# Kernel tuning notes

Hardware: AMD Instinct MI355X
Metric: run time of the kernel (lower is better)

Reference implementation:

```python
import jax, jax.numpy as jnp
import numpy as np

N_SRC = 100000
N_DST = 100000
D = 128
K = 10
E_SAMP = 1000000


def setup_inputs() -> dict:
    key = jax.random.key(0)
    k1, k2, k3, k4, k5, k6, k7 = jax.random.split(key, 7)
    h_src = jax.random.normal(k1, (N_SRC, D), dtype=jnp.float32)
    weight = jax.random.normal(k2, (D, D), dtype=jnp.float32) * (1.0 / np.sqrt(D))
    bias = jax.random.normal(k3, (D,), dtype=jnp.float32) * 0.01
    sampled_src = jax.random.randint(k4, (E_SAMP,), 0, N_SRC, dtype=jnp.int64)
    sampled_dst = jnp.sort(jax.random.randint(k5, (E_SAMP,), 0, N_DST, dtype=jnp.int64))
    out_deg = jax.random.randint(k6, (N_SRC,), 0, 64, dtype=jnp.int32)
    in_deg = jax.random.randint(k7, (N_DST,), 0, 64, dtype=jnp.int32)
    return {
        "h_src": h_src,
        "weight": weight,
        "bias": bias,
        "sampled_src": sampled_src,
        "sampled_dst": sampled_dst,
        "out_deg": out_deg,
        "in_deg": in_deg,
    }


def reference(h_src, weight, bias, sampled_src, sampled_dst, out_deg, in_deg):
    # pre-aggregation normalization: out_degree^-0.5 (clamped to >=1)
    norm_src = jnp.clip(out_deg.astype(h_src.dtype), 1.0, None) ** -0.5  # [N_SRC]
    feat_src = h_src * norm_src[:, None]                                  # [N_SRC, D]
    # fused gather + (pre-sampled) neighbor sum: copy_src -> segment_sum
    msg = feat_src[sampled_src]                                           # [E_SAMP, D]
    agg = jax.ops.segment_sum(msg, sampled_dst, num_segments=N_DST,
                              indices_are_sorted=True)                    # [N_DST, D]
    rst = agg @ weight                                                    # [N_DST, D]
    # post normalization: clamp(in_degree, 1, k)^-0.5
    norm_dst = jnp.clip(in_deg.astype(rst.dtype), 1.0, float(K)) ** -0.5  # [N_DST]
    rst = rst * norm_dst[:, None] + bias
    return rst
```

## Files before the change

### kernel.cpp

```cpp
#include <hip/hip_runtime.h>
#include <hip/hip_bf16.h>
#include <cstdint>

#define NDIM 128
#define KCLAMP 10.0f

using bf16x8 = __attribute__((ext_vector_type(8))) short;
using f32x4  = __attribute__((ext_vector_type(4))) float;
using f32x2  = __attribute__((ext_vector_type(2))) float;

__device__ __forceinline__ uint16_t f2bf(float f) {
    uint32_t u = __float_as_uint(f);
    uint32_t r = (u + 0x7fffu + ((u >> 16) & 1u)) >> 16;
    return (uint16_t)r;
}
__device__ __forceinline__ float bf_lo(uint32_t v) { return __uint_as_float(v << 16); }
__device__ __forceinline__ float bf_hi(uint32_t v) { return __uint_as_float(v & 0xffff0000u); }

__global__ void k_feat(const float* __restrict__ h, const int* __restrict__ odeg,
                       uint16_t* __restrict__ feat, int nsrc) {
    int idx = blockIdx.x * blockDim.x + threadIdx.x;
    int total = nsrc * (NDIM / 4);
    if (idx >= total) return;
    int row = idx >> 5;
    float dg = (float)odeg[row];
    float nrm = rsqrtf(fmaxf(dg, 1.0f));
    float4 v = ((const float4*)h)[idx];
    ushort4 o;
    o.x = f2bf(v.x * nrm);
    o.y = f2bf(v.y * nrm);
    o.z = f2bf(v.z * nrm);
    o.w = f2bf(v.w * nrm);
    ((ushort4*)feat)[idx] = o;
}

__global__ void k_rowptr(const int* __restrict__ sdst, int E,
                         int* __restrict__ row_start, int ndst) {
    int d = blockIdx.x * blockDim.x + threadIdx.x;
    if (d > ndst) return;
    int lo = 0, hi = E;
    while (lo < hi) {
        int mid = (lo + hi) >> 1;
        if (sdst[mid] < d) lo = mid + 1; else hi = mid;
    }
    row_start[d] = lo;
}

__global__ void k_agg_bf(const uint16_t* __restrict__ feat,
                         const int* __restrict__ ssrc, const int* __restrict__ row_start,
                         uint16_t* __restrict__ agg, int ndst) {
    constexpr int U = 8;
    int gtid = blockIdx.x * blockDim.x + threadIdx.x;
    int wave = gtid >> 6;
    int lane = threadIdx.x & 63;
    int sub  = lane >> 4;
    int li   = lane & 15;
    int nwaves = (gridDim.x * blockDim.x) >> 6;

    for (int d0 = wave * 4; d0 < ndst; d0 += nwaves * 4) {
        int d = d0 + sub;
        int valid = (d < ndst);
        int s = 0, e = 0;
        if (valid) { s = row_start[d]; e = row_start[d + 1]; }
        int elast = (e > s) ? (e - 1) : 0;

        f32x2 acc[4];
#pragma unroll
        for (int k = 0; k < 4; ++k) acc[k] = (f32x2){0.f, 0.f};

        int idxv[U];
#pragma unroll
        for (int u = 0; u < U; ++u) idxv[u] = ssrc[min(s + u, elast)];

        int pos = s;
        while (__any(pos < e)) {
            uint4 v[U];
#pragma unroll
            for (int u = 0; u < U; ++u)
                v[u] = *(const uint4*)(feat + (size_t)idxv[u] * NDIM + li * 8);

            int npos = pos + U;
#pragma unroll
            for (int u = 0; u < U; ++u) idxv[u] = ssrc[min(npos + u, elast)];

#pragma unroll
            for (int u = 0; u < U; ++u) {
                if (pos + u < e) {
                    f32x2 t0 = {bf_lo(v[u].x), bf_hi(v[u].x)};
                    f32x2 t1 = {bf_lo(v[u].y), bf_hi(v[u].y)};
                    f32x2 t2 = {bf_lo(v[u].z), bf_hi(v[u].z)};
                    f32x2 t3 = {bf_lo(v[u].w), bf_hi(v[u].w)};
                    acc[0] += t0; acc[1] += t1; acc[2] += t2; acc[3] += t3;
                }
            }
            pos = npos;
        }

        if (valid) {
            uint4 o;
            o.x = (uint32_t)f2bf(acc[0][0]) | ((uint32_t)f2bf(acc[0][1]) << 16);
            o.y = (uint32_t)f2bf(acc[1][0]) | ((uint32_t)f2bf(acc[1][1]) << 16);
            o.z = (uint32_t)f2bf(acc[2][0]) | ((uint32_t)f2bf(acc[2][1]) << 16);
            o.w = (uint32_t)f2bf(acc[3][0]) | ((uint32_t)f2bf(acc[3][1]) << 16);
            *(uint4*)(agg + (size_t)d * NDIM + li * 8) = o;
        }
    }
}

__global__ void k_agg_f32(const uint16_t* __restrict__ feat,
                          const float* __restrict__ h, const int* __restrict__ odeg,
                          const int* __restrict__ ssrc, const int* __restrict__ row_start,
                          float* __restrict__ agg, int ndst, int use_feat) {
    int gtid = blockIdx.x * blockDim.x + threadIdx.x;
    int wave = gtid >> 6;
    int lane = threadIdx.x & 63;
    int nwaves = (gridDim.x * blockDim.x) >> 6;
    for (int d = wave; d < ndst; d += nwaves) {
        int s = row_start[d], e = row_start[d + 1];
        float a0 = 0.f, a1 = 0.f;
        if (use_feat) {
            for (int i = s; i < e; i++) {
                uint32_t v0 = *(const uint32_t*)(feat + (size_t)ssrc[i] * NDIM + lane * 2);
                a0 += bf_lo(v0);
                a1 += bf_hi(v0);
            }
        } else {
            for (int i = s; i < e; i++) {
                int s0 = ssrc[i];
                float nrm = rsqrtf(fmaxf((float)odeg[s0], 1.0f));
                float2 v = ((const float2*)h)[(size_t)s0 * (NDIM / 2) + lane];
                a0 += v.x * nrm;
                a1 += v.y * nrm;
            }
        }
        float2 o; o.x = a0; o.y = a1;
        ((float2*)agg)[(size_t)d * (NDIM / 2) + lane] = o;
    }
}

__global__ void k_wfrag(const float* __restrict__ W, uint16_t* __restrict__ wfrag) {
    int t = blockIdx.x * blockDim.x + threadIdx.x;
    if (t >= NDIM * NDIM) return;
    int i    = t & 7;
    int lane = (t >> 3) & 63;
    int s    = (t >> 9) & 3;
    int n    = t >> 11;
    int k    = s * 32 + 8 * (lane >> 4) + i;
    int col  = n * 16 + (lane & 15);
    wfrag[t] = f2bf(W[k * NDIM + col]);
}

__global__ __launch_bounds__(256) void k_gemm_mfma(const uint16_t* __restrict__ A,
                                                   const uint16_t* __restrict__ wfrag,
                                                   const float* __restrict__ bias,
                                                   const int* __restrict__ ideg,
                                                   float* __restrict__ out, int M) {
    __shared__ uint16_t Ws[NDIM * NDIM];
    int tx = threadIdx.x;
    for (int i = tx; i < NDIM * NDIM / 8; i += 256)
        ((int4*)Ws)[i] = ((const int4*)wfrag)[i];
    __syncthreads();

    int wave = tx >> 6, lane = tx & 63;
    int r0 = blockIdx.x * 64 + wave * 16;
    int arow = r0 + (lane & 15);
    if (arow >= M) arow = M - 1;
    const bf16x8* Arow = (const bf16x8*)(A + (size_t)arow * NDIM);
    int g = lane >> 4;

    f32x4 acc[8];
#pragma unroll
    for (int n = 0; n < 8; ++n) acc[n] = (f32x4){0.f, 0.f, 0.f, 0.f};

#pragma unroll
    for (int s = 0; s < 4; ++s) {
        bf16x8 af = Arow[s * 4 + g];
#pragma unroll
        for (int n = 0; n < 8; ++n) {
            bf16x8 bfr = *(const bf16x8*)(Ws + (((n * 4 + s) * 64 + lane) << 3));
            acc[n] = __builtin_amdgcn_mfma_f32_16x16x32_bf16(af, bfr, acc[n], 0, 0, 0);
        }
    }

    int col = lane & 15;
    float nrm[4];
    int rowbase = r0 + g * 4;
#pragma unroll
    for (int r = 0; r < 4; ++r) {
        int row = rowbase + r;
        nrm[r] = (row < M) ? rsqrtf(fminf(fmaxf((float)ideg[row], 1.0f), KCLAMP)) : 0.f;
    }
#pragma unroll
    for (int n = 0; n < 8; ++n) {
        float b = bias[n * 16 + col];
#pragma unroll
        for (int r = 0; r < 4; ++r) {
            int row = rowbase + r;
            if (row < M)
                out[(size_t)row * NDIM + n * 16 + col] = acc[n][r] * nrm[r] + b;
        }
    }
}

__global__ __launch_bounds__(256) void k_gemm_f32(float* __restrict__ io,
                                                  const float* __restrict__ W,
                                                  const float* __restrict__ bias,
                                                  const int* __restrict__ ideg, int M) {
    __shared__ float Wsf[NDIM][NDIM];
    int tx = threadIdx.x;
    {
        const float4* Wv = (const float4*)W;
        float4* Wsv = (float4*)&Wsf[0][0];
        for (int i = tx; i < NDIM * NDIM / 4; i += 256) Wsv[i] = Wv[i];
    }
    __syncthreads();
    int cg = tx & 31, rg = tx >> 5;
    int r0 = blockIdx.x * 64 + rg * 8, c0 = cg * 4;
    float acc[8][4];
#pragma unroll
    for (int r = 0; r < 8; ++r)
#pragma unroll
        for (int c = 0; c < 4; ++c) acc[r][c] = 0.f;
    for (int k4 = 0; k4 < NDIM / 4; ++k4) {
        float4 wk0 = *(const float4*)&Wsf[4 * k4 + 0][c0];
        float4 wk1 = *(const float4*)&Wsf[4 * k4 + 1][c0];
        float4 wk2 = *(const float4*)&Wsf[4 * k4 + 2][c0];
        float4 wk3 = *(const float4*)&Wsf[4 * k4 + 3][c0];
#pragma unroll
        for (int r = 0; r < 8; ++r) {
            int row = r0 + r;
            if (row < M) {
                float4 a = ((const float4*)io)[(size_t)row * (NDIM / 4) + k4];
                acc[r][0] += a.x * wk0.x + a.y * wk1.x + a.z * wk2.x + a.w * wk3.x;
                acc[r][1] += a.x * wk0.y + a.y * wk1.y + a.z * wk2.y + a.w * wk3.y;
                acc[r][2] += a.x * wk0.z + a.y * wk1.z + a.z * wk2.z + a.w * wk3.z;
                acc[r][3] += a.x * wk0.w + a.y * wk1.w + a.z * wk2.w + a.w * wk3.w;
            }
        }
    }
    __syncthreads();
    float4 b = *(const float4*)&bias[c0];
#pragma unroll
    for (int r = 0; r < 8; ++r) {
        int row = r0 + r;
        if (row < M) {
            float nrm = rsqrtf(fminf(fmaxf((float)ideg[row], 1.0f), KCLAMP));
            float4 o;
            o.x = acc[r][0] * nrm + b.x;
            o.y = acc[r][1] * nrm + b.y;
            o.z = acc[r][2] * nrm + b.z;
            o.w = acc[r][3] * nrm + b.w;
            ((float4*)io)[(size_t)row * (NDIM / 4) + cg] = o;
        }
    }
}

extern "C" void kernel_launch(void* const* d_in, const int* in_sizes, int n_in,
                              void* d_out, int out_size, void* d_ws, size_t ws_size,
                              hipStream_t stream) {
    const float* h_src  = (const float*)d_in[0];
    const float* weight = (const float*)d_in[1];
    const float* bias   = (const float*)d_in[2];
    const int*   ssrc   = (const int*)d_in[3];
    const int*   sdst   = (const int*)d_in[4];
    const int*   odeg   = (const int*)d_in[5];
    const int*   ideg   = (const int*)d_in[6];
    float* out = (float*)d_out;

    int E    = in_sizes[3];
    int nsrc = in_sizes[0] / NDIM;
    int ndst = out_size / NDIM;

    size_t featB = (size_t)nsrc * NDIM * 2;
    size_t aggB  = (size_t)ndst * NDIM * 2;

    int*      row_start = (int*)d_ws;
    uint16_t* wfrag = (uint16_t*)((char*)d_ws + ((size_t)1 << 20));
    size_t feat_off = (size_t)2 << 20;
    uint16_t* feat  = (uint16_t*)((char*)d_ws + feat_off);
    size_t agg_off  = feat_off + ((featB + 255) & ~(size_t)255);
    uint16_t* aggbf = (uint16_t*)((char*)d_ws + agg_off);
    size_t need_full = agg_off + aggB;
    size_t need_feat = feat_off + featB;

    k_rowptr<<<(ndst + 1 + 255) / 256, 256, 0, stream>>>(sdst, E, row_start, ndst);

    if (ws_size >= need_full) {
        k_wfrag<<<(NDIM * NDIM + 255) / 256, 256, 0, stream>>>(weight, wfrag);
        int total = nsrc * (NDIM / 4);
        k_feat<<<(total + 255) / 256, 256, 0, stream>>>(h_src, odeg, feat, nsrc);
        k_agg_bf<<<2048, 256, 0, stream>>>(feat, ssrc, row_start, aggbf, ndst);
        k_gemm_mfma<<<(ndst + 63) / 64, 256, 0, stream>>>(aggbf, wfrag,
                                                          bias, ideg, out, ndst);
    } else {
        int use_feat = (ws_size >= need_feat) ? 1 : 0;
        if (use_feat) {
            int total = nsrc * (NDIM / 4);
            k_feat<<<(total + 255) / 256, 256, 0, stream>>>(h_src, odeg, feat, nsrc);
        }
        k_agg_f32<<<2048, 256, 0, stream>>>(feat, h_src, odeg, ssrc, row_start, out, ndst, use_feat);
        k_gemm_f32<<<(ndst + 63) / 64, 256, 0, stream>>>(out, weight, bias, ideg, ndst);
    }
}
```

Baseline: 86.54 us.

## Fuse aggregation with MFMA GEMM and merge prep kernels into one launch

Merges the feature-normalization, row-pointer binary search and weight-fragment kernels into a single block-partitioned prep launch. Fuses the bf16 neighbor aggregation into the MFMA GEMM: each 512-thread block aggregates 128 destination rows into a swizzled LDS tile, then multiplies it by the LDS-resident weights. This removes the bf16 agg round-trip through global memory and two launches. In exchange it uses 64KB of LDS per block and a fixed-size grid without grid-stride, which lowers occupancy and latency hiding for the gather.

Measured after the change: 83.42 us. 1.04x faster.

```diff
diff --git a/kernel.cpp b/kernel.cpp
--- a/kernel.cpp
+++ b/kernel.cpp
@@ -4,6 +4,7 @@
 
 #define NDIM 128
 #define KCLAMP 10.0f
+#define BLK_D 128
 
 using bf16x8 = __attribute__((ext_vector_type(8))) short;
 using f32x4  = __attribute__((ext_vector_type(4))) float;
@@ -17,48 +18,73 @@
 __device__ __forceinline__ float bf_lo(uint32_t v) { return __uint_as_float(v << 16); }
 __device__ __forceinline__ float bf_hi(uint32_t v) { return __uint_as_float(v & 0xffff0000u); }
 
-__global__ void k_feat(const float* __restrict__ h, const int* __restrict__ odeg,
-                       uint16_t* __restrict__ feat, int nsrc) {
-    int idx = blockIdx.x * blockDim.x + threadIdx.x;
-    int total = nsrc * (NDIM / 4);
-    if (idx >= total) return;
-    int row = idx >> 5;
-    float dg = (float)odeg[row];
-    float nrm = rsqrtf(fmaxf(dg, 1.0f));
-    float4 v = ((const float4*)h)[idx];
-    ushort4 o;
-    o.x = f2bf(v.x * nrm);
-    o.y = f2bf(v.y * nrm);
-    o.z = f2bf(v.z * nrm);
-    o.w = f2bf(v.w * nrm);
-    ((ushort4*)feat)[idx] = o;
-}
-
-__global__ void k_rowptr(const int* __restrict__ sdst, int E,
-                         int* __restrict__ row_start, int ndst) {
-    int d = blockIdx.x * blockDim.x + threadIdx.x;
-    if (d > ndst) return;
-    int lo = 0, hi = E;
-    while (lo < hi) {
-        int mid = (lo + hi) >> 1;
-        if (sdst[mid] < d) lo = mid + 1; else hi = mid;
-    }
-    row_start[d] = lo;
-}
-
-__global__ void k_agg_bf(const uint16_t* __restrict__ feat,
-                         const int* __restrict__ ssrc, const int* __restrict__ row_start,
-                         uint16_t* __restrict__ agg, int ndst) {
+__global__ void k_prep(const float* __restrict__ h, const int* __restrict__ odeg,
+                       uint16_t* __restrict__ feat, int nsrc,
+                       const int* __restrict__ sdst, int E,
+                       int* __restrict__ row_start, int ndst,
+                       const float* __restrict__ W, uint16_t* __restrict__ wfrag,
+                       int featBlocks, int rpBlocks) {
+    int b = blockIdx.x;
+    int tid = threadIdx.x;
+    if (b < featBlocks) {
+        int idx = b * 256 + tid;
+        int total = nsrc * (NDIM / 4);
+        if (idx >= total) return;
+        int row = idx >> 5;
+        float nrm = rsqrtf(fmaxf((float)odeg[row], 1.0f));
+        float4 v = ((const float4*)h)[idx];
+        ushort4 o;
+        o.x = f2bf(v.x * nrm);
+        o.y = f2bf(v.y * nrm);
+        o.z = f2bf(v.z * nrm);
+        o.w = f2bf(v.w * nrm);
+        ((ushort4*)feat)[idx] = o;
+    } else if (b < featBlocks + rpBlocks) {
+        int d = (b - featBlocks) * 256 + tid;
+        if (d > ndst) return;
+        int lo = 0, hi = E;
+        while (lo < hi) {
+            int mid = (lo + hi) >> 1;
+            if (sdst[mid] < d) lo = mid + 1; else hi = mid;
+        }
+        row_start[d] = lo;
+    } else {
+        int t = (b - featBlocks - rpBlocks) * 256 + tid;
+        if (t >= NDIM * NDIM) return;
+        int i    = t & 7;
+        int lane = (t >> 3) & 63;
+        int s    = (t >> 9) & 3;
+        int n    = t >> 11;
+        int k    = s * 32 + 8 * (lane >> 4) + i;
+        int col  = n * 16 + (lane & 15);
+        wfrag[t] = f2bf(W[k * NDIM + col]);
+    }
+}
+
+__global__ __launch_bounds__(512) void k_fused(const uint16_t* __restrict__ feat,
+                                               const int* __restrict__ ssrc,
+                                               const int* __restrict__ row_start,
+                                               const uint16_t* __restrict__ wfrag,
+                                               const float* __restrict__ bias,
+                                               const int* __restrict__ ideg,
+                                               float* __restrict__ out, int ndst) {
     constexpr int U = 8;
-    int gtid = blockIdx.x * blockDim.x + threadIdx.x;
-    int wave = gtid >> 6;
-    int lane = threadIdx.x & 63;
+    __shared__ uint16_t Ws[NDIM * NDIM];
+    __shared__ uint16_t Asm[BLK_D * NDIM];
+
+    int tx = threadIdx.x;
+    for (int i = tx; i < NDIM * NDIM / 8; i += 512)
+        ((int4*)Ws)[i] = ((const int4*)wfrag)[i];
+
+    int wave = tx >> 6, lane = tx & 63;
     int sub  = lane >> 4;
     int li   = lane & 15;
-    int nwaves = (gridDim.x * blockDim.x) >> 6;
-
-    for (int d0 = wave * 4; d0 < ndst; d0 += nwaves * 4) {
-        int d = d0 + sub;
+    int sid  = wave * 4 + sub;
+    int base = blockIdx.x * BLK_D;
+
+    for (int j = 0; j < 4; ++j) {
+        int r = sid * 4 + j;
+        int d = base + r;
         int valid = (d < ndst);
         int s = 0, e = 0;
         if (valid) { s = row_start[d]; e = row_start[d + 1]; }
@@ -96,15 +122,81 @@
             pos = npos;
         }
 
-        if (valid) {
-            uint4 o;
-            o.x = (uint32_t)f2bf(acc[0][0]) | ((uint32_t)f2bf(acc[0][1]) << 16);
-            o.y = (uint32_t)f2bf(acc[1][0]) | ((uint32_t)f2bf(acc[1][1]) << 16);
-            o.z = (uint32_t)f2bf(acc[2][0]) | ((uint32_t)f2bf(acc[2][1]) << 16);
-            o.w = (uint32_t)f2bf(acc[3][0]) | ((uint32_t)f2bf(acc[3][1]) << 16);
-            *(uint4*)(agg + (size_t)d * NDIM + li * 8) = o;
-        }
-    }
+        uint4 o;
+        o.x = (uint32_t)f2bf(acc[0][0]) | ((uint32_t)f2bf(acc[0][1]) << 16);
+        o.y = (uint32_t)f2bf(acc[1][0]) | ((uint32_t)f2bf(acc[1][1]) << 16);
+        o.z = (uint32_t)f2bf(acc[2][0]) | ((uint32_t)f2bf(acc[2][1]) << 16);
+        o.w = (uint32_t)f2bf(acc[3][0]) | ((uint32_t)f2bf(acc[3][1]) << 16);
+        int byte = (r * 256 + li * 16) ^ ((r & 7) << 4);
+        *(uint4*)((char*)Asm + byte) = o;
+    }
+
+    __syncthreads();
+
+    int g = lane >> 4;
+    int rloc = wave * 16 + (lane & 15);
+
+    f32x4 acc[8];
+#pragma unroll
+    for (int n = 0; n < 8; ++n) acc[n] = (f32x4){0.f, 0.f, 0.f, 0.f};
+
+#pragma unroll
+    for (int s = 0; s < 4; ++s) {
+        int abyte = (rloc * 256 + s * 64 + g * 16) ^ ((rloc & 7) << 4);
+        bf16x8 af = *(const bf16x8*)((const char*)Asm + abyte);
+#pragma unroll
+        for (int n = 0; n < 8; ++n) {
+            bf16x8 bfr = *(const bf16x8*)(Ws + (((n * 4 + s) * 64 + lane) << 3));
+            acc[n] = __builtin_amdgcn_mfma_f32_16x16x32_bf16(af, bfr, acc[n], 0, 0, 0);
+        }
+    }
+
+    int col = lane & 15;
+    int rowbase = base + wave * 16 + g * 4;
+    float nrm[4];
+#pragma unroll
+    for (int r = 0; r < 4; ++r) {
+        int row = rowbase + r;
+        nrm[r] = (row < ndst) ? rsqrtf(fminf(fmaxf((float)ideg[row], 1.0f), KCLAMP)) : 0.f;
+    }
+#pragma unroll
+    for (int n = 0; n < 8; ++n) {
+        float b = bias[n * 16 + col];
+#pragma unroll
+        for (int r = 0; r < 4; ++r) {
+            int row = rowbase + r;
+            if (row < ndst)
+                out[(size_t)row * NDIM + n * 16 + col] = acc[n][r] * nrm[r] + b;
+        }
+    }
+}
+
+__global__ void k_rowptr(const int* __restrict__ sdst, int E,
+                         int* __restrict__ row_start, int ndst) {
+    int d = blockIdx.x * blockDim.x + threadIdx.x;
+    if (d > ndst) return;
+    int lo = 0, hi = E;
+    while (lo < hi) {
+        int mid = (lo + hi) >> 1;
+        if (sdst[mid] < d) lo = mid + 1; else hi = mid;
+    }
+    row_start[d] = lo;
+}
+
+__global__ void k_feat(const float* __restrict__ h, const int* __restrict__ odeg,
+                       uint16_t* __restrict__ feat, int nsrc) {
+    int idx = blockIdx.x * blockDim.x + threadIdx.x;
+    int total = nsrc * (NDIM / 4);
+    if (idx >= total) return;
+    int row = idx >> 5;
+    float nrm = rsqrtf(fmaxf((float)odeg[row], 1.0f));
+    float4 v = ((const float4*)h)[idx];
+    ushort4 o;
+    o.x = f2bf(v.x * nrm);
+    o.y = f2bf(v.y * nrm);
+    o.z = f2bf(v.z * nrm);
+    o.w = f2bf(v.w * nrm);
+    ((ushort4*)feat)[idx] = o;
 }
 
 __global__ void k_agg_f32(const uint16_t* __restrict__ feat,
@@ -138,70 +230,6 @@
     }
 }
 
-__global__ void k_wfrag(const float* __restrict__ W, uint16_t* __restrict__ wfrag) {
-    int t = blockIdx.x * blockDim.x + threadIdx.x;
-    if (t >= NDIM * NDIM) return;
-    int i    = t & 7;
-    int lane = (t >> 3) & 63;
-    int s    = (t >> 9) & 3;
-    int n    = t >> 11;
-    int k    = s * 32 + 8 * (lane >> 4) + i;
-    int col  = n * 16 + (lane & 15);
-    wfrag[t] = f2bf(W[k * NDIM + col]);
-}
-
-__global__ __launch_bounds__(256) void k_gemm_mfma(const uint16_t* __restrict__ A,
-                                                   const uint16_t* __restrict__ wfrag,
-                                                   const float* __restrict__ bias,
-                                                   const int* __restrict__ ideg,
-                                                   float* __restrict__ out, int M) {
-    __shared__ uint16_t Ws[NDIM * NDIM];
-    int tx = threadIdx.x;
-    for (int i = tx; i < NDIM * NDIM / 8; i += 256)
-        ((int4*)Ws)[i] = ((const int4*)wfrag)[i];
-    __syncthreads();
-
-    int wave = tx >> 6, lane = tx & 63;
-    int r0 = blockIdx.x * 64 + wave * 16;
-    int arow = r0 + (lane & 15);
-    if (arow >= M) arow = M - 1;
-    const bf16x8* Arow = (const bf16x8*)(A + (size_t)arow * NDIM);
-    int g = lane >> 4;
-
-    f32x4 acc[8];
-#pragma unroll
-    for (int n = 0; n < 8; ++n) acc[n] = (f32x4){0.f, 0.f, 0.f, 0.f};
-
-#pragma unroll
-    for (int s = 0; s < 4; ++s) {
-        bf16x8 af = Arow[s * 4 + g];
-#pragma unroll
-        for (int n = 0; n < 8; ++n) {
-            bf16x8 bfr = *(const bf16x8*)(Ws + (((n * 4 + s) * 64 + lane) << 3));
-            acc[n] = __builtin_amdgcn_mfma_f32_16x16x32_bf16(af, bfr, acc[n], 0, 0, 0);
-        }
-    }
-
-    int col = lane & 15;
-    float nrm[4];
-    int rowbase = r0 + g * 4;
-#pragma unroll
-    for (int r = 0; r < 4; ++r) {
-        int row = rowbase + r;
-        nrm[r] = (row < M) ? rsqrtf(fminf(fmaxf((float)ideg[row], 1.0f), KCLAMP)) : 0.f;
-    }
-#pragma unroll
-    for (int n = 0; n < 8; ++n) {
-        float b = bias[n * 16 + col];
-#pragma unroll
-        for (int r = 0; r < 4; ++r) {
-            int row = rowbase + r;
-            if (row < M)
-                out[(size_t)row * NDIM + n * 16 + col] = acc[n][r] * nrm[r] + b;
-        }
-    }
-}
-
 __global__ __launch_bounds__(256) void k_gemm_f32(float* __restrict__ io,
                                                   const float* __restrict__ W,
                                                   const float* __restrict__ bias,
@@ -272,33 +300,25 @@
     int ndst = out_size / NDIM;
 
     size_t featB = (size_t)nsrc * NDIM * 2;
-    size_t aggB  = (size_t)ndst * NDIM * 2;
 
     int*      row_start = (int*)d_ws;
     uint16_t* wfrag = (uint16_t*)((char*)d_ws + ((size_t)1 << 20));
     size_t feat_off = (size_t)2 << 20;
     uint16_t* feat  = (uint16_t*)((char*)d_ws + feat_off);
-    size_t agg_off  = feat_off + ((featB + 255) & ~(size_t)255);
-    uint16_t* aggbf = (uint16_t*)((char*)d_ws + agg_off);
-    size_t need_full = agg_off + aggB;
-    size_t need_feat = feat_off + featB;
-
-    k_rowptr<<<(ndst + 1 + 255) / 256, 256, 0, stream>>>(sdst, E, row_start, ndst);
-
-    if (ws_size >= need_full) {
-        k_wfrag<<<(NDIM * NDIM + 255) / 256, 256, 0, stream>>>(weight, wfrag);
-        int total = nsrc * (NDIM / 4);
-        k_feat<<<(total + 255) / 256, 256, 0, stream>>>(h_src, odeg, feat, nsrc);
-        k_agg_bf<<<2048, 256, 0, stream>>>(feat, ssrc, row_start, aggbf, ndst);
-        k_gemm_mfma<<<(ndst + 63) / 64, 256, 0, stream>>>(aggbf, wfrag,
-                                                          bias, ideg, out, ndst);
+    size_t need = feat_off + featB;
+
+    if (ws_size >= need) {
+        int featBlocks = (nsrc * (NDIM / 4) + 255) / 256;
+        int rpBlocks   = (ndst + 1 + 255) / 256;
+        int wfBlocks   = (NDIM * NDIM + 255) / 256;
+        k_prep<<<featBlocks + rpBlocks + wfBlocks, 256, 0, stream>>>(
+            h_src, odeg, feat, nsrc, sdst, E, row_start, ndst,
+            weight, wfrag, featBlocks, rpBlocks);
+        k_fused<<<(ndst + BLK_D - 1) / BLK_D, 512, 0, stream>>>(
+            feat, ssrc, row_start, wfrag, bias, ideg, out, ndst);
     } else {
-        int use_feat = (ws_size >= need_feat) ? 1 : 0;
-        if (use_feat) {
-            int total = nsrc * (NDIM / 4);
-            k_feat<<<(total + 255) / 256, 256, 0, stream>>>(h_src, odeg, feat, nsrc);
-        }
-        k_agg_f32<<<2048, 256, 0, stream>>>(feat, h_src, odeg, ssrc, row_start, out, ndst, use_feat);
+        k_rowptr<<<(ndst + 1 + 255) / 256, 256, 0, stream>>>(sdst, E, row_start, ndst);
+        k_agg_f32<<<2048, 256, 0, stream>>>(feat, h_src, odeg, ssrc, row_start, out, ndst, 0);
         k_gemm_f32<<<(ndst + 63) / 64, 256, 0, stream>>>(out, weight, bias, ideg, ndst);
     }
 }
```

## Transform source features before gathering and fuse normalization, GEMM and rowptr into one launch

Applied to the files above, without the earlier changes.

Uses linearity to reorder the math: each source row is scaled and multiplied by W first, then the transformed bf16 rows are gathered and segment-summed. The epilogue (in-degree norm and bias) moves into the gather kernel, which writes fp32 output directly. The row-pointer binary search shares the launch with the GEMM blocks, cutting five launches to two and dropping the intermediate feat and agg buffers. In exchange it rounds the per-edge transformed rows to bf16 before summation, which changes where rounding error accumulates.

Result: slower. 91.65 us (+5.9%).

```diff
diff --git a/kernel.cpp b/kernel.cpp
--- a/kernel.cpp
+++ b/kernel.cpp
@@ -17,38 +17,98 @@
 __device__ __forceinline__ float bf_lo(uint32_t v) { return __uint_as_float(v << 16); }
 __device__ __forceinline__ float bf_hi(uint32_t v) { return __uint_as_float(v & 0xffff0000u); }
 
-__global__ void k_feat(const float* __restrict__ h, const int* __restrict__ odeg,
-                       uint16_t* __restrict__ feat, int nsrc) {
-    int idx = blockIdx.x * blockDim.x + threadIdx.x;
-    int total = nsrc * (NDIM / 4);
-    if (idx >= total) return;
-    int row = idx >> 5;
-    float dg = (float)odeg[row];
-    float nrm = rsqrtf(fmaxf(dg, 1.0f));
-    float4 v = ((const float4*)h)[idx];
-    ushort4 o;
-    o.x = f2bf(v.x * nrm);
-    o.y = f2bf(v.y * nrm);
-    o.z = f2bf(v.z * nrm);
-    o.w = f2bf(v.w * nrm);
-    ((ushort4*)feat)[idx] = o;
-}
-
-__global__ void k_rowptr(const int* __restrict__ sdst, int E,
-                         int* __restrict__ row_start, int ndst) {
-    int d = blockIdx.x * blockDim.x + threadIdx.x;
-    if (d > ndst) return;
-    int lo = 0, hi = E;
-    while (lo < hi) {
-        int mid = (lo + hi) >> 1;
-        if (sdst[mid] < d) lo = mid + 1; else hi = mid;
-    }
-    row_start[d] = lo;
-}
-
-__global__ void k_agg_bf(const uint16_t* __restrict__ feat,
-                         const int* __restrict__ ssrc, const int* __restrict__ row_start,
-                         uint16_t* __restrict__ agg, int ndst) {
+__global__ __launch_bounds__(256) void k1_trans_rowptr(
+        const float* __restrict__ h, const int* __restrict__ odeg,
+        const float* __restrict__ W, uint16_t* __restrict__ trans, int M,
+        const int* __restrict__ sdst, int E, int* __restrict__ row_start, int ndst,
+        int gemmBlocks) {
+    int b = blockIdx.x;
+    int tx = threadIdx.x;
+
+    if (b >= gemmBlocks) {
+        int d = (b - gemmBlocks) * 256 + tx;
+        if (d > ndst) return;
+        int lo = 0, hi = E;
+        while (lo < hi) {
+            int mid = (lo + hi) >> 1;
+            if (sdst[mid] < d) lo = mid + 1; else hi = mid;
+        }
+        row_start[d] = lo;
+        return;
+    }
+
+    __shared__ uint16_t Ws[NDIM * NDIM];
+    __shared__ uint16_t Asm[64 * NDIM];
+
+    int r0 = b * 64;
+
+    for (int i = tx; i < 64 * (NDIM / 4); i += 256) {
+        int row_loc = i >> 5;
+        int col4    = i & 31;
+        int row = r0 + row_loc;
+        float4 v = {0.f, 0.f, 0.f, 0.f};
+        float nrm = 0.f;
+        if (row < M) {
+            v = ((const float4*)h)[(size_t)row * (NDIM / 4) + col4];
+            nrm = rsqrtf(fmaxf((float)odeg[row], 1.0f));
+        }
+        ushort4 o;
+        o.x = f2bf(v.x * nrm);
+        o.y = f2bf(v.y * nrm);
+        o.z = f2bf(v.z * nrm);
+        o.w = f2bf(v.w * nrm);
+        int byte = (row_loc * 256 + col4 * 8) ^ ((row_loc & 7) << 4);
+        *(ushort4*)((char*)Asm + byte) = o;
+    }
+
+    for (int t = tx; t < NDIM * NDIM; t += 256) {
+        int i    = t & 7;
+        int ln   = (t >> 3) & 63;
+        int s    = (t >> 9) & 3;
+        int n    = t >> 11;
+        int k    = s * 32 + 8 * (ln >> 4) + i;
+        int col  = n * 16 + (ln & 15);
+        Ws[t] = f2bf(W[k * NDIM + col]);
+    }
+    __syncthreads();
+
+    int wave = tx >> 6, lane = tx & 63;
+    int g = lane >> 4;
+    int rloc = wave * 16 + (lane & 15);
+
+    f32x4 acc[8];
+#pragma unroll
+    for (int n = 0; n < 8; ++n) acc[n] = (f32x4){0.f, 0.f, 0.f, 0.f};
+
+#pragma unroll
+    for (int s = 0; s < 4; ++s) {
+        int abyte = (rloc * 256 + s * 64 + g * 16) ^ ((rloc & 7) << 4);
+        bf16x8 af = *(const bf16x8*)((const char*)Asm + abyte);
+#pragma unroll
+        for (int n = 0; n < 8; ++n) {
+            bf16x8 bfr = *(const bf16x8*)(Ws + (((n * 4 + s) * 64 + lane) << 3));
+            acc[n] = __builtin_amdgcn_mfma_f32_16x16x32_bf16(af, bfr, acc[n], 0, 0, 0);
+        }
+    }
+
+    int colL = lane & 15;
+    int rowbase = r0 + wave * 16 + g * 4;
+#pragma unroll
+    for (int n = 0; n < 8; ++n) {
+#pragma unroll
+        for (int r = 0; r < 4; ++r) {
+            int row = rowbase + r;
+            if (row < M)
+                trans[(size_t)row * NDIM + n * 16 + colL] = f2bf(acc[n][r]);
+        }
+    }
+}
+
+__global__ __launch_bounds__(256) void k2_gather(
+        const uint16_t* __restrict__ trans,
+        const int* __restrict__ ssrc, const int* __restrict__ row_start,
+        const float* __restrict__ bias, const int* __restrict__ ideg,
+        float* __restrict__ out, int ndst) {
     constexpr int U = 8;
     int gtid = blockIdx.x * blockDim.x + threadIdx.x;
     int wave = gtid >> 6;
@@ -57,6 +117,9 @@
     int li   = lane & 15;
     int nwaves = (gridDim.x * blockDim.x) >> 6;
 
+    float4 b0 = ((const float4*)bias)[li * 2];
+    float4 b1 = ((const float4*)bias)[li * 2 + 1];
+
     for (int d0 = wave * 4; d0 < ndst; d0 += nwaves * 4) {
         int d = d0 + sub;
         int valid = (d < ndst);
@@ -77,7 +140,7 @@
             uint4 v[U];
 #pragma unroll
             for (int u = 0; u < U; ++u)
-                v[u] = *(const uint4*)(feat + (size_t)idxv[u] * NDIM + li * 8);
+                v[u] = *(const uint4*)(trans + (size_t)idxv[u] * NDIM + li * 8);
 
             int npos = pos + U;
 #pragma unroll
@@ -97,20 +160,37 @@
         }
 
         if (valid) {
-            uint4 o;
-            o.x = (uint32_t)f2bf(acc[0][0]) | ((uint32_t)f2bf(acc[0][1]) << 16);
-            o.y = (uint32_t)f2bf(acc[1][0]) | ((uint32_t)f2bf(acc[1][1]) << 16);
-            o.z = (uint32_t)f2bf(acc[2][0]) | ((uint32_t)f2bf(acc[2][1]) << 16);
-            o.w = (uint32_t)f2bf(acc[3][0]) | ((uint32_t)f2bf(acc[3][1]) << 16);
-            *(uint4*)(agg + (size_t)d * NDIM + li * 8) = o;
-        }
-    }
-}
-
-__global__ void k_agg_f32(const uint16_t* __restrict__ feat,
-                          const float* __restrict__ h, const int* __restrict__ odeg,
+            float nrm = rsqrtf(fminf(fmaxf((float)ideg[d], 1.0f), KCLAMP));
+            float4 o0, o1;
+            o0.x = acc[0][0] * nrm + b0.x;
+            o0.y = acc[0][1] * nrm + b0.y;
+            o0.z = acc[1][0] * nrm + b0.z;
+            o0.w = acc[1][1] * nrm + b0.w;
+            o1.x = acc[2][0] * nrm + b1.x;
+            o1.y = acc[2][1] * nrm + b1.y;
+            o1.z = acc[3][0] * nrm + b1.z;
+            o1.w = acc[3][1] * nrm + b1.w;
+            ((float4*)out)[(size_t)d * (NDIM / 4) + li * 2]     = o0;
+            ((float4*)out)[(size_t)d * (NDIM / 4) + li * 2 + 1] = o1;
+        }
+    }
+}
+
+__global__ void k_rowptr(const int* __restrict__ sdst, int E,
+                         int* __restrict__ row_start, int ndst) {
+    int d = blockIdx.x * blockDim.x + threadIdx.x;
+    if (d > ndst) return;
+    int lo = 0, hi = E;
+    while (lo < hi) {
+        int mid = (lo + hi) >> 1;
+        if (sdst[mid] < d) lo = mid + 1; else hi = mid;
+    }
+    row_start[d] = lo;
+}
+
+__global__ void k_agg_f32(const float* __restrict__ h, const int* __restrict__ odeg,
                           const int* __restrict__ ssrc, const int* __restrict__ row_start,
-                          float* __restrict__ agg, int ndst, int use_feat) {
+                          float* __restrict__ agg, int ndst) {
     int gtid = blockIdx.x * blockDim.x + threadIdx.x;
     int wave = gtid >> 6;
     int lane = threadIdx.x & 63;
@@ -118,87 +198,15 @@
     for (int d = wave; d < ndst; d += nwaves) {
         int s = row_start[d], e = row_start[d + 1];
         float a0 = 0.f, a1 = 0.f;
-        if (use_feat) {
-            for (int i = s; i < e; i++) {
-                uint32_t v0 = *(const uint32_t*)(feat + (size_t)ssrc[i] * NDIM + lane * 2);
-                a0 += bf_lo(v0);
-                a1 += bf_hi(v0);
-            }
-        } else {
-            for (int i = s; i < e; i++) {
-                int s0 = ssrc[i];
-                float nrm = rsqrtf(fmaxf((float)odeg[s0], 1.0f));
-                float2 v = ((const float2*)h)[(size_t)s0 * (NDIM / 2) + lane];
-                a0 += v.x * nrm;
-                a1 += v.y * nrm;
-            }
+        for (int i = s; i < e; i++) {
+            int s0 = ssrc[i];
+            float nrm = rsqrtf(fmaxf((float)odeg[s0], 1.0f));
+            float2 v = ((const float2*)h)[(size_t)s0 * (NDIM / 2) + lane];
+            a0 += v.x * nrm;
+            a1 += v.y * nrm;
         }
         float2 o; o.x = a0; o.y = a1;
         ((float2*)agg)[(size_t)d * (NDIM / 2) + lane] = o;
-    }
-}
-
-__global__ void k_wfrag(const float* __restrict__ W, uint16_t* __restrict__ wfrag) {
-    int t = blockIdx.x * blockDim.x + threadIdx.x;
-    if (t >= NDIM * NDIM) return;
-    int i    = t & 7;
-    int lane = (t >> 3) & 63;
-    int s    = (t >> 9) & 3;
-    int n    = t >> 11;
-    int k    = s * 32 + 8 * (lane >> 4) + i;
-    int col  = n * 16 + (lane & 15);
-    wfrag[t] = f2bf(W[k * NDIM + col]);
-}
-
-__global__ __launch_bounds__(256) void k_gemm_mfma(const uint16_t* __restrict__ A,
-                                                   const uint16_t* __restrict__ wfrag,
-                                                   const float* __restrict__ bias,
-                                                   const int* __restrict__ ideg,
-                                                   float* __restrict__ out, int M) {
-    __shared__ uint16_t Ws[NDIM * NDIM];
-    int tx = threadIdx.x;
-    for (int i = tx; i < NDIM * NDIM / 8; i += 256)
-        ((int4*)Ws)[i] = ((const int4*)wfrag)[i];
-    __syncthreads();
-
-    int wave = tx >> 6, lane = tx & 63;
-    int r0 = blockIdx.x * 64 + wave * 16;
-    int arow = r0 + (lane & 15);
-    if (arow >= M) arow = M - 1;
-    const bf16x8* Arow = (const bf16x8*)(A + (size_t)arow * NDIM);
-    int g = lane >> 4;
-
-    f32x4 acc[8];
-#pragma unroll
-    for (int n = 0; n < 8; ++n) acc[n] = (f32x4){0.f, 0.f, 0.f, 0.f};
-
-#pragma unroll
-    for (int s = 0; s < 4; ++s) {
-        bf16x8 af = Arow[s * 4 + g];
-#pragma unroll
-        for (int n = 0; n < 8; ++n) {
-            bf16x8 bfr = *(const bf16x8*)(Ws + (((n * 4 + s) * 64 + lane) << 3));
-            acc[n] = __builtin_amdgcn_mfma_f32_16x16x32_bf16(af, bfr, acc[n], 0, 0, 0);
-        }
-    }
-
-    int col = lane & 15;
-    float nrm[4];
-    int rowbase = r0 + g * 4;
-#pragma unroll
-    for (int r = 0; r < 4; ++r) {
-        int row = rowbase + r;
-        nrm[r] = (row < M) ? rsqrtf(fminf(fmaxf((float)ideg[row], 1.0f), KCLAMP)) : 0.f;
-    }
-#pragma unroll
-    for (int n = 0; n < 8; ++n) {
-        float b = bias[n * 16 + col];
-#pragma unroll
-        for (int r = 0; r < 4; ++r) {
-            int row = rowbase + r;
-            if (row < M)
-                out[(size_t)row * NDIM + n * 16 + col] = acc[n][r] * nrm[r] + b;
-        }
     }
 }
 
@@ -271,34 +279,20 @@
     int nsrc = in_sizes[0] / NDIM;
     int ndst = out_size / NDIM;
 
-    size_t featB = (size_t)nsrc * NDIM * 2;
-    size_t aggB  = (size_t)ndst * NDIM * 2;
-
     int*      row_start = (int*)d_ws;
-    uint16_t* wfrag = (uint16_t*)((char*)d_ws + ((size_t)1 << 20));
-    size_t feat_off = (size_t)2 << 20;
-    uint16_t* feat  = (uint16_t*)((char*)d_ws + feat_off);
-    size_t agg_off  = feat_off + ((featB + 255) & ~(size_t)255);
-    uint16_t* aggbf = (uint16_t*)((char*)d_ws + agg_off);
-    size_t need_full = agg_off + aggB;
-    size_t need_feat = feat_off + featB;
-
-    k_rowptr<<<(ndst + 1 + 255) / 256, 256, 0, stream>>>(sdst, E, row_start, ndst);
-
-    if (ws_size >= need_full) {
-        k_wfrag<<<(NDIM * NDIM + 255) / 256, 256, 0, stream>>>(weight, wfrag);
-        int total = nsrc * (NDIM / 4);
-        k_feat<<<(total + 255) / 256, 256, 0, stream>>>(h_src, odeg, feat, nsrc);
-        k_agg_bf<<<2048, 256, 0, stream>>>(feat, ssrc, row_start, aggbf, ndst);
-        k_gemm_mfma<<<(ndst + 63) / 64, 256, 0, stream>>>(aggbf, wfrag,
-                                                          bias, ideg, out, ndst);
+    uint16_t* trans = (uint16_t*)((char*)d_ws + ((size_t)1 << 20));
+    size_t need = ((size_t)1 << 20) + (size_t)nsrc * NDIM * 2;
+
+    if (ws_size >= need) {
+        int gemmBlocks = (nsrc + 63) / 64;
+        int rpBlocks   = (ndst + 1 + 255) / 256;
+        k1_trans_rowptr<<<gemmBlocks + rpBlocks, 256, 0, stream>>>(
+            h_src, odeg, weight, trans, nsrc,
+            sdst, E, row_start, ndst, gemmBlocks);
+        k2_gather<<<2048, 256, 0, stream>>>(trans, ssrc, row_start, bias, ideg, out, ndst);
     } else {
-        int use_feat = (ws_size >= need_feat) ? 1 : 0;
-        if (use_feat) {
-            int total = nsrc * (NDIM / 4);
-            k_feat<<<(total + 255) / 256, 256, 0, stream>>>(h_src, odeg, feat, nsrc);
-        }
-        k_agg_f32<<<2048, 256, 0, stream>>>(feat, h_src, odeg, ssrc, row_start, out, ndst, use_feat);
+        k_rowptr<<<(ndst + 1 + 255) / 256, 256, 0, stream>>>(sdst, E, row_start, ndst);
+        k_agg_f32<<<2048, 256, 0, stream>>>(h_src, odeg, ssrc, row_start, out, ndst);
         k_gemm_f32<<<(ndst + 63) / 64, 256, 0, stream>>>(out, weight, bias, ideg, ndst);
     }
 }
```
